# Kernel optimization log

Hardware: AMD Instinct MI355X
Metric: run time of the kernel (lower is better)

## Reference

```python
import jax, jax.numpy as jnp
import numpy as np

B_CAPS = 32   # number of capsule types
K = 3         # kernel size
P = 4         # pose matrix side
STRIDE = 2
ITERS = 3
PSIZE = P * P
LN_2PI = np.float32(np.log(2.0 * np.pi))


def setup_inputs() -> dict:
    key = jax.random.key(0)
    k1, k2, k3, k4, k5 = jax.random.split(key, 5)
    b, h, w = 32, 32, 32
    x = jax.random.normal(k1, (b, h, w, B_CAPS, PSIZE), jnp.float32)
    a = jax.random.uniform(k2, (b, h, w, B_CAPS, 1), jnp.float32)
    # learned params (torch: weights (1,1,1,K*K,B,P,P), beta_u/beta_a (B,1))
    weights = jax.random.normal(k3, (K * K, B_CAPS, P, P), jnp.float32)
    beta_u = 0.1 * jax.random.normal(k4, (B_CAPS, 1), jnp.float32)
    beta_a = 0.1 * jax.random.normal(k5, (B_CAPS, 1), jnp.float32)
    return {"x": x, "a": a, "weights": weights, "beta_u": beta_u, "beta_a": beta_a}


def _patch(t):
    # t: (b, h, w, B, psize) -> (b, oh, ow, K*K, B, psize)
    b, h, w = t.shape[0], t.shape[1], t.shape[2]
    starts = np.arange(0, h - K + 1, STRIDE)
    idxs = starts[:, None] + np.arange(K)[None, :]          # (oh, K) static gather indices
    oh = idxs.shape[0]
    t = t[:, idxs]                                           # (b, oh, K, w, B, ps)
    t = t[:, :, :, idxs]                                     # (b, oh, K, ow, K, B, ps)
    t = jnp.transpose(t, (0, 1, 3, 2, 4, 5, 6))              # (b, oh, ow, K, K, B, ps)
    return t.reshape(b, oh, oh, K * K, t.shape[-2], t.shape[-1]), oh


def _em_routing(v, a_in, beta_u, beta_a):
    # v: (b,h,w,Bk,C,psize)  a_in: (b,h,w,Bk,C)   Bk = K*K, C = B_CAPS
    eps = 1e-6
    lam = 1e-3
    b, h, w, Bk, C, ps = v.shape
    mu = sigma_sq = a_out = None
    for it in range(ITERS):
        if it == 0:
            r = a_in / C                                                    # (b,h,w,Bk,C)
        else:
            ln_pjh = (-(v - mu) ** 2 / (2.0 * sigma_sq)
                      - jnp.log(jnp.sqrt(sigma_sq)) - 0.5 * LN_2PI)         # (b,h,w,Bk,C,ps)
            ln_ap = ln_pjh.sum(axis=5) + jnp.log(a_out.reshape(b, h, w, 1, C))
            r = jax.nn.softmax(ln_ap, axis=4)
        r_sum = r.sum(axis=3, keepdims=True)                                # (b,h,w,1,C)
        coeff = (r / (r_sum + eps))[..., None]                              # (b,h,w,Bk,C,1)
        mu = jnp.sum(coeff * v, axis=3, keepdims=True)                      # (b,h,w,1,C,ps)
        sigma_sq = jnp.sum(coeff * (v - mu) ** 2, axis=3, keepdims=True) + eps
        cost_h = (beta_u + jnp.log(jnp.sqrt(sigma_sq))) * r_sum[..., None]  # (b,h,w,1,C,ps)
        a_out = jax.nn.sigmoid(lam * (beta_a - cost_h.sum(axis=5, keepdims=True)))
    return mu.reshape(b, h, w, C, ps), a_out.reshape(b, h, w, C, 1)


def reference(x, a, weights, beta_u, beta_a):
    b = x.shape[0]
    p_in, oh = _patch(x)                                    # (b,oh,ow,K*K,B,psize)
    a_in, _ = _patch(a)                                     # (b,oh,ow,K*K,B,1)
    p = p_in.reshape(b, oh, oh, K * K, B_CAPS, P, P)
    # voting: per-window, per-type 4x4 pose matmul
    v = jnp.einsum('bhwkcpq,kcqr->bhwkcpr', p, weights).reshape(b, oh, oh, K * K, B_CAPS, PSIZE)
    a_in = a_in.reshape(b, oh, oh, K * K, B_CAPS)
    return _em_routing(v, a_in, beta_u, beta_a)
```

## Files before the change

### kernel.cpp

```cpp
#include <hip/hip_runtime.h>
#include <math.h>

#define PP 9
#define CAPS 32
#define PS 16
#define OH 15
#define HH 32
#define WW 32
#define LN_2PI 1.8378770664093453f

__device__ __forceinline__ float frcp(float x) {
    float r;
    asm("v_rcp_f32 %0, %1" : "=v"(r) : "v"(x));
    return r;
}

template <int CTRL>
__device__ __forceinline__ float dppf(float x) {
    int r = __builtin_amdgcn_update_dpp(0, __builtin_bit_cast(int, x), CTRL, 0xF, 0xF, true);
    return __builtin_bit_cast(float, r);
}
__device__ __forceinline__ float row_sum16(float x) {
    x += dppf<0xB1>(x);
    x += dppf<0x4E>(x);
    x += dppf<0x124>(x);
    x += dppf<0x128>(x);
    return x;
}
__device__ __forceinline__ float row_max16(float x) {
    x = fmaxf(x, dppf<0xB1>(x));
    x = fmaxf(x, dppf<0x4E>(x));
    x = fmaxf(x, dppf<0x124>(x));
    x = fmaxf(x, dppf<0x128>(x));
    return x;
}
__device__ __forceinline__ float swz_xor16(float x) {
    return __builtin_bit_cast(float,
        __builtin_amdgcn_ds_swizzle(__builtin_bit_cast(int, x), 0x401F));
}

__global__ __launch_bounds__(64, 2) void emcaps_kernel(
    const float* __restrict__ x,
    const float* __restrict__ a,
    const float* __restrict__ wgt,
    const float* __restrict__ beta_u,
    const float* __restrict__ beta_a,
    float* __restrict__ out_mu,
    float* __restrict__ out_a)
{
    const int lane = threadIdx.x;
    const int s = lane >> 5;
    const int c = lane & 31;

    const int site = blockIdx.x * 2 + s;
    const int j = site % OH;
    const int t2 = site / OH;
    const int i = t2 % OH;
    const int b = t2 / OH;
    const int h0 = 2 * i, w0 = 2 * j;

    float v[PP][PS];
    float r[PP];
    #pragma unroll
    for (int k = 0; k < PP; ++k) {
        const int hh = h0 + k / 3, ww = w0 + k % 3;
        const size_t pix = (size_t)(b * HH + hh) * WW + ww;
        const float* xb = x + pix * (CAPS * PS) + c * PS;
        *(float4*)&v[k][0]  = *(const float4*)xb;
        *(float4*)&v[k][4]  = *(const float4*)(xb + 4);
        *(float4*)&v[k][8]  = *(const float4*)(xb + 8);
        *(float4*)&v[k][12] = *(const float4*)(xb + 12);
        r[k] = a[pix * CAPS + c] * (1.f / 32.f);
    }

    #pragma unroll
    for (int k = 0; k < PP; ++k) {
        float xt[PS], wl[PS];
        #pragma unroll
        for (int t = 0; t < PS; ++t) xt[t] = v[k][t];
        const float* wb = wgt + k * (CAPS * PS) + c * PS;
        *(float4*)&wl[0]  = *(const float4*)wb;
        *(float4*)&wl[4]  = *(const float4*)(wb + 4);
        *(float4*)&wl[8]  = *(const float4*)(wb + 8);
        *(float4*)&wl[12] = *(const float4*)(wb + 12);
        #pragma unroll
        for (int t = 0; t < PS; ++t) {
            float acc = 0.f;
            #pragma unroll
            for (int q = 0; q < 4; ++q)
                acc = fmaf(xt[(t & 12) + q], wl[q * 4 + (t & 3)], acc);
            v[k][t] = acc;
        }
    }

    const float bu = beta_u[c];
    const float ba = beta_a[c];
    const float eps = 1e-6f;
    const float lam = 1e-3f;

    float mu[PS], sig[PS];
    float aoc = 0.f;
    float slgfull = 0.f;
    float r_sum;

    for (int it = 0; it < 3; ++it) {
        if (it > 0) {
            const float addc = __logf(aoc) - slgfull - 8.f * LN_2PI;
            float inv2s[PS];
            #pragma unroll
            for (int t = 0; t < PS; ++t) inv2s[t] = frcp(2.f * sig[t]);
            #pragma unroll
            for (int k = 0; k < PP; ++k) {
                float sacc = 0.f;
                #pragma unroll
                for (int t = 0; t < PS; ++t) {
                    float d = v[k][t] - mu[t];
                    sacc = fmaf(d * d, inv2s[t], sacc);
                }
                const float lnk = addc - sacc;
                float mx = row_max16(lnk);
                mx = fmaxf(mx, swz_xor16(mx));
                float e = __expf(lnk - mx);
                float ss = row_sum16(e);
                ss += swz_xor16(ss);
                r[k] = e * frcp(ss);
            }
        }

        r_sum = 0.f;
        #pragma unroll
        for (int k = 0; k < PP; ++k) r_sum += r[k];
        const float invr = frcp(r_sum + eps);
        #pragma unroll
        for (int k = 0; k < PP; ++k) r[k] *= invr;

        #pragma unroll
        for (int t = 0; t < PS; ++t) {
            float m = 0.f;
            #pragma unroll
            for (int k = 0; k < PP; ++k) m = fmaf(r[k], v[k][t], m);
            mu[t] = m;
        }
        float slg = 0.f;
        #pragma unroll
        for (int t = 0; t < PS; ++t) {
            float sacc = 0.f;
            #pragma unroll
            for (int k = 0; k < PP; ++k) {
                float d = v[k][t] - mu[t];
                sacc = fmaf(r[k] * d, d, sacc);
            }
            sig[t] = sacc + eps;
            slg += 0.5f * __logf(sig[t]);
        }
        slgfull = slg;
        const float ch = r_sum * (16.f * bu + slgfull);
        aoc = frcp(1.f + __expf(-lam * (ba - ch)));
    }

    float* ob = out_mu + (size_t)site * (CAPS * PS) + c * PS;
    *(float4*)(ob + 0)  = make_float4(mu[0],  mu[1],  mu[2],  mu[3]);
    *(float4*)(ob + 4)  = make_float4(mu[4],  mu[5],  mu[6],  mu[7]);
    *(float4*)(ob + 8)  = make_float4(mu[8],  mu[9],  mu[10], mu[11]);
    *(float4*)(ob + 12) = make_float4(mu[12], mu[13], mu[14], mu[15]);
    out_a[(size_t)site * CAPS + c] = aoc;
}

extern "C" void kernel_launch(void* const* d_in, const int* in_sizes, int n_in,
                              void* d_out, int out_size, void* d_ws, size_t ws_size,
                              hipStream_t stream) {
    const float* x      = (const float*)d_in[0];
    const float* a      = (const float*)d_in[1];
    const float* wgt    = (const float*)d_in[2];
    const float* beta_u = (const float*)d_in[3];
    const float* beta_a = (const float*)d_in[4];

    float* out_mu = (float*)d_out;
    float* out_a  = (float*)d_out + (size_t)32 * OH * OH * CAPS * PS;

    const int n_sites = 32 * OH * OH;
    emcaps_kernel<<<n_sites / 2, 64, 0, stream>>>(x, a, wgt, beta_u, beta_a, out_mu, out_a);
}
```

Measured before the change: 39.74 us.

## Split each site's pose dimension across two half-waves to halve per-thread registers

Each 64-lane block now handles a single output site instead of two. The two 32-lane halves each own 8 of the 16 pose elements, so per-thread vote and mean/variance storage is roughly halved and twice as many waves are launched. Per-capsule partial sums (the Gaussian log-likelihood and the log-sigma total) are combined across halves with a lane-xor-32 shuffle, and launch bounds are raised to allow more resident waves. The cost is routing and softmax work repeated in both halves, plus extra cross-lane shuffles per routing step.

```diff
diff --git a/kernel.cpp b/kernel.cpp
--- a/kernel.cpp
+++ b/kernel.cpp
@@ -4,6 +4,7 @@
 #define PP 9
 #define CAPS 32
 #define PS 16
+#define HPS 8
 #define OH 15
 #define HH 32
 #define WW 32
@@ -38,8 +39,11 @@
     return __builtin_bit_cast(float,
         __builtin_amdgcn_ds_swizzle(__builtin_bit_cast(int, x), 0x401F));
 }
+__device__ __forceinline__ float xhalf(float x) {
+    return __shfl_xor(x, 32);
+}
 
-__global__ __launch_bounds__(64, 2) void emcaps_kernel(
+__global__ __launch_bounds__(64, 4) void emcaps_kernel(
     const float* __restrict__ x,
     const float* __restrict__ a,
     const float* __restrict__ wgt,
@@ -49,47 +53,46 @@
     float* __restrict__ out_a)
 {
     const int lane = threadIdx.x;
-    const int s = lane >> 5;
+    const int half = lane >> 5;
     const int c = lane & 31;
 
-    const int site = blockIdx.x * 2 + s;
+    const int site = blockIdx.x;
     const int j = site % OH;
     const int t2 = site / OH;
     const int i = t2 % OH;
     const int b = t2 / OH;
     const int h0 = 2 * i, w0 = 2 * j;
 
-    float v[PP][PS];
+    float v[PP][HPS];
     float r[PP];
     #pragma unroll
     for (int k = 0; k < PP; ++k) {
         const int hh = h0 + k / 3, ww = w0 + k % 3;
         const size_t pix = (size_t)(b * HH + hh) * WW + ww;
-        const float* xb = x + pix * (CAPS * PS) + c * PS;
-        *(float4*)&v[k][0]  = *(const float4*)xb;
-        *(float4*)&v[k][4]  = *(const float4*)(xb + 4);
-        *(float4*)&v[k][8]  = *(const float4*)(xb + 8);
-        *(float4*)&v[k][12] = *(const float4*)(xb + 12);
+        const float* xb = x + pix * (CAPS * PS) + c * PS + half * HPS;
+        *(float4*)&v[k][0] = *(const float4*)xb;
+        *(float4*)&v[k][4] = *(const float4*)(xb + 4);
         r[k] = a[pix * CAPS + c] * (1.f / 32.f);
     }
 
     #pragma unroll
     for (int k = 0; k < PP; ++k) {
-        float xt[PS], wl[PS];
+        float xt[HPS];
         #pragma unroll
-        for (int t = 0; t < PS; ++t) xt[t] = v[k][t];
+        for (int u = 0; u < HPS; ++u) xt[u] = v[k][u];
+        float wl[PS];
         const float* wb = wgt + k * (CAPS * PS) + c * PS;
         *(float4*)&wl[0]  = *(const float4*)wb;
         *(float4*)&wl[4]  = *(const float4*)(wb + 4);
         *(float4*)&wl[8]  = *(const float4*)(wb + 8);
         *(float4*)&wl[12] = *(const float4*)(wb + 12);
         #pragma unroll
-        for (int t = 0; t < PS; ++t) {
+        for (int u = 0; u < HPS; ++u) {
             float acc = 0.f;
             #pragma unroll
             for (int q = 0; q < 4; ++q)
-                acc = fmaf(xt[(t & 12) + q], wl[q * 4 + (t & 3)], acc);
-            v[k][t] = acc;
+                acc = fmaf(xt[(u & 4) + q], wl[q * 4 + (u & 3)], acc);
+            v[k][u] = acc;
         }
     }
 
@@ -98,7 +101,7 @@
     const float eps = 1e-6f;
     const float lam = 1e-3f;
 
-    float mu[PS], sig[PS];
+    float mu[HPS], is2[HPS];
     float aoc = 0.f;
     float slgfull = 0.f;
     float r_sum;
@@ -106,17 +109,15 @@
     for (int it = 0; it < 3; ++it) {
         if (it > 0) {
             const float addc = __logf(aoc) - slgfull - 8.f * LN_2PI;
-            float inv2s[PS];
-            #pragma unroll
-            for (int t = 0; t < PS; ++t) inv2s[t] = frcp(2.f * sig[t]);
             #pragma unroll
             for (int k = 0; k < PP; ++k) {
                 float sacc = 0.f;
                 #pragma unroll
-                for (int t = 0; t < PS; ++t) {
-                    float d = v[k][t] - mu[t];
-                    sacc = fmaf(d * d, inv2s[t], sacc);
+                for (int u = 0; u < HPS; ++u) {
+                    float d = v[k][u] - mu[u];
+                    sacc = fmaf(d * d, is2[u], sacc);
                 }
+                sacc += xhalf(sacc);
                 const float lnk = addc - sacc;
                 float mx = row_max16(lnk);
                 mx = fmaxf(mx, swz_xor16(mx));
@@ -135,35 +136,34 @@
         for (int k = 0; k < PP; ++k) r[k] *= invr;
 
         #pragma unroll
-        for (int t = 0; t < PS; ++t) {
+        for (int u = 0; u < HPS; ++u) {
             float m = 0.f;
             #pragma unroll
-            for (int k = 0; k < PP; ++k) m = fmaf(r[k], v[k][t], m);
-            mu[t] = m;
+            for (int k = 0; k < PP; ++k) m = fmaf(r[k], v[k][u], m);
+            mu[u] = m;
         }
         float slg = 0.f;
         #pragma unroll
-        for (int t = 0; t < PS; ++t) {
+        for (int u = 0; u < HPS; ++u) {
             float sacc = 0.f;
             #pragma unroll
             for (int k = 0; k < PP; ++k) {
-                float d = v[k][t] - mu[t];
+                float d = v[k][u] - mu[u];
                 sacc = fmaf(r[k] * d, d, sacc);
             }
-            sig[t] = sacc + eps;
-            slg += 0.5f * __logf(sig[t]);
+            const float sg = sacc + eps;
+            is2[u] = frcp(2.f * sg);
+            slg += 0.5f * __logf(sg);
         }
-        slgfull = slg;
+        slgfull = slg + xhalf(slg);
         const float ch = r_sum * (16.f * bu + slgfull);
         aoc = frcp(1.f + __expf(-lam * (ba - ch)));
     }
 
-    float* ob = out_mu + (size_t)site * (CAPS * PS) + c * PS;
-    *(float4*)(ob + 0)  = make_float4(mu[0],  mu[1],  mu[2],  mu[3]);
-    *(float4*)(ob + 4)  = make_float4(mu[4],  mu[5],  mu[6],  mu[7]);
-    *(float4*)(ob + 8)  = make_float4(mu[8],  mu[9],  mu[10], mu[11]);
-    *(float4*)(ob + 12) = make_float4(mu[12], mu[13], mu[14], mu[15]);
-    out_a[(size_t)site * CAPS + c] = aoc;
+    float* ob = out_mu + (size_t)site * (CAPS * PS) + c * PS + half * HPS;
+    *(float4*)(ob + 0) = make_float4(mu[0], mu[1], mu[2], mu[3]);
+    *(float4*)(ob + 4) = make_float4(mu[4], mu[5], mu[6], mu[7]);
+    if (half == 0) out_a[(size_t)site * CAPS + c] = aoc;
 }
 
 extern "C" void kernel_launch(void* const* d_in, const int* in_sizes, int n_in,
@@ -179,5 +179,5 @@
     float* out_a  = (float*)d_out + (size_t)32 * OH * OH * CAPS * PS;
 
     const int n_sites = 32 * OH * OH;
-    emcaps_kernel<<<n_sites / 2, 64, 0, stream>>>(x, a, wgt, beta_u, beta_a, out_mu, out_a);
+    emcaps_kernel<<<n_sites, 64, 0, stream>>>(x, a, wgt, beta_u, beta_a, out_mu, out_a);
 }
```

Result: slower. 44.96 us (+13.1%).
